# Kernel tuning notes

Hardware: AMD Instinct MI355X
Metric: run time of the kernel (lower is better)

Reference implementation:

```python
import itertools
import jax, jax.numpy as jnp
import numpy as np

N = 400000
CIN, COUT = 32, 64
K, STRIDE, PAD, DIL = 3, 2, 1, 1
SPATIAL = (200, 200, 16)
PRUNING_RATIO = 0.5

def _out_spatial():
    return tuple((s + 2 * PAD - DIL * (K - 1) - 1) // STRIDE + 1 for s in SPATIAL)


def setup_inputs() -> dict:
    key = jax.random.key(0)
    kf, kc0, kc1, kc2, kc3, km, kw = jax.random.split(key, 7)
    features = jax.random.normal(kf, (N, CIN), dtype=jnp.float32)
    b = jax.random.randint(kc0, (N,), 0, 2, dtype=jnp.int32)
    z = jax.random.randint(kc1, (N,), 0, SPATIAL[0], dtype=jnp.int32)
    y = jax.random.randint(kc2, (N,), 0, SPATIAL[1], dtype=jnp.int32)
    x = jax.random.randint(kc3, (N,), 0, SPATIAL[2], dtype=jnp.int32)
    coors = jnp.stack([b, z, y, x], axis=1)  # [N,4] = (batch, d0, d1, d2)
    mask = jax.random.uniform(km, (N,), dtype=jnp.float32)
    weight = jax.random.normal(kw, (K, K, K, CIN, COUT), dtype=jnp.float32) * 0.05
    return {"features": features, "coors": coors, "mask": mask, "weight": weight, "batch_size": 2}


def _sprs_conv(features, coors, mask, weight, batch_size):
    out_sp = _out_spatial()  # (100, 100, 8)
    num_out = batch_size * out_sp[0] * out_sp[1] * out_sp[2]
    n = features.shape[0]
    # rank-based pruning: keep top (1 - pruning_ratio) points as 'important'
    thr = jnp.sort(mask)[int(n * PRUNING_RATIO)]
    important = (mask >= thr)  # [N] bool

    b = coors[:, 0]
    pos = coors[:, 1:4]  # [N,3]
    out_sp_arr = jnp.array(out_sp, dtype=pos.dtype)

    # accumulators; slot num_out is a dump for invalid indices
    acc = jnp.zeros((num_out + 1, COUT), dtype=features.dtype)
    imp_cnt = jnp.zeros((num_out + 1,), dtype=jnp.int32)

    for off in itertools.product(range(K), repeat=3):
        off_arr = jnp.array(off, dtype=pos.dtype)
        num = pos + PAD - DIL * off_arr  # [N,3]
        oc = num // STRIDE
        valid = jnp.all(num % STRIDE == 0, axis=-1) & jnp.all(oc >= 0, axis=-1) & jnp.all(oc < out_sp_arr, axis=-1)
        lin = ((b * out_sp[0] + oc[:, 0]) * out_sp[1] + oc[:, 1]) * out_sp[2] + oc[:, 2]
        idx = jnp.where(valid, lin, num_out)
        vals = features @ weight[off[0], off[1], off[2]]  # [N,Cout] gather-GEMM
        acc = acc.at[idx].add(vals)  # scatter
        imp_cnt = imp_cnt.at[idx].add((important & valid).astype(jnp.int32))

    keep = (imp_cnt[:num_out] > 0)  # output positions reached by >=1 important point
    return acc[:num_out] * keep[:, None]


def reference(features, coors, mask, weight, batch_size):
    return _sprs_conv(features, coors, mask, weight, batch_size)
```

## Files before the change

### kernel.cpp

```cpp
#include <hip/hip_runtime.h>

#define CIN 32
#define COUT 64
#define OD0 100
#define OD1 100
#define OD2 8
#define IZ 200
#define IY 200
#define IX 16
#define NTAP 27
#define NCELLS (2 * IZ * IY * IX)
#define TOY 4
#define TOX 8
#define NROW 27
#define NCELL_R (NROW * 16)
#define NBIN 12
#define CAPB 80
#define CAPF 176


__global__ void hist0_fused_kernel(const float* __restrict__ mask, const int* __restrict__ coors,
                                   const float* __restrict__ W, int n,
                                   int* __restrict__ hist, int* __restrict__ S,
                                   float* __restrict__ Wt) {
    __shared__ int h[256];
    h[threadIdx.x] = 0;
    __syncthreads();
    for (int i = blockIdx.x * blockDim.x + threadIdx.x; i < n; i += gridDim.x * blockDim.x) {
        unsigned bits = __float_as_uint(mask[i]);
        atomicAdd(&h[bits >> 24], 1);
        const int4 c = ((const int4*)coors)[i];
        int cell = ((c.x * IZ + c.y) * IY + c.z) * IX + c.w;
        atomicAdd(&S[cell], 1);
    }
    for (int i = blockIdx.x * blockDim.x + threadIdx.x; i < NTAP * CIN * COUT;
         i += gridDim.x * blockDim.x) {
        int cout = i % COUT;
        int rest = i / COUT;
        int cin = rest % CIN;
        int tap = rest / CIN;
        Wt[((size_t)tap * COUT + cout) * CIN + cin] = W[i];
    }
    __syncthreads();
    int v = h[threadIdx.x];
    if (v) atomicAdd(&hist[threadIdx.x], v);
}

__global__ void hist8_kernel(const float* __restrict__ mask, int n, int level,
                             const int* __restrict__ state, int* __restrict__ hist) {
    __shared__ int h[256];
    h[threadIdx.x] = 0;
    __syncthreads();
    unsigned pfx = (unsigned)state[0];
    int sh = 24 - 8 * level;
    for (int i = blockIdx.x * blockDim.x + threadIdx.x; i < n; i += gridDim.x * blockDim.x) {
        unsigned bits = __float_as_uint(mask[i]);
        if ((bits >> (sh + 8)) == pfx)
            atomicAdd(&h[(bits >> sh) & 0xFF], 1);
    }
    __syncthreads();
    int v = h[threadIdx.x];
    if (v) atomicAdd(&hist[threadIdx.x], v);
}

__global__ void select8_kernel(const int* __restrict__ hist, int* __restrict__ state,
                               int level, int rankConst) {
    __shared__ int sc[256];
    sc[threadIdx.x] = hist[threadIdx.x];
    __syncthreads();
    if (threadIdx.x == 0) {
        int rank = level ? state[1] : rankConst;
        unsigned pfx = level ? (unsigned)state[0] : 0u;
        int c = 0;
        for (int j = 0; j < 256; j++) {
            int hv = sc[j];
            if (rank < c + hv) {
                state[0] = (int)((pfx << 8) | (unsigned)j);
                state[1] = rank - c;
                break;
            }
            c += hv;
        }
    }
}


__global__ void scan_l0_kernel(int* __restrict__ S, int* __restrict__ partials) {
    __shared__ int ts[256];
    int tid = threadIdx.x;
    int4 v = ((int4*)S)[blockIdx.x * 256 + tid];
    int s1 = v.x + v.y, s2 = s1 + v.z, s3 = s2 + v.w;
    ts[tid] = s3;
    __syncthreads();
    for (int off = 1; off < 256; off <<= 1) {
        int t = (tid >= off) ? ts[tid - off] : 0;
        __syncthreads();
        ts[tid] += t;
        __syncthreads();
    }
    int excl = ts[tid] - s3;
    int4 o;
    o.x = excl; o.y = excl + v.x; o.z = excl + s1; o.w = excl + s2;
    ((int4*)S)[blockIdx.x * 256 + tid] = o;
    if (tid == 255) partials[blockIdx.x] = ts[255];
}

__global__ void scan_l1_kernel(int* __restrict__ partials, int nP) {
    __shared__ int sums[256];
    int tid = threadIdx.x;
    int per = (nP + 255) / 256;
    int lo = tid * per, hi = lo + per;
    if (hi > nP) hi = nP;
    int s = 0;
    for (int j = lo; j < hi; j++) s += partials[j];
    sums[tid] = s;
    __syncthreads();
    for (int off = 1; off < 256; off <<= 1) {
        int t = (tid >= off) ? sums[tid - off] : 0;
        __syncthreads();
        sums[tid] += t;
        __syncthreads();
    }
    int run = sums[tid] - s;
    for (int j = lo; j < hi; j++) { int v = partials[j]; partials[j] = run; run += v; }
}

__global__ void scan_l2_kernel(int* __restrict__ S, const int* __restrict__ partials) {
    int add = partials[blockIdx.x];
    if (add == 0) return;
    int4 v = ((int4*)S)[blockIdx.x * 256 + threadIdx.x];
    v.x += add; v.y += add; v.z += add; v.w += add;
    ((int4*)S)[blockIdx.x * 256 + threadIdx.x] = v;
}

__global__ void scatter_points_kernel(const int* __restrict__ coors, const float* __restrict__ mask,
                                      const int* __restrict__ state, int n,
                                      int* __restrict__ S, int* __restrict__ entries) {
    int i = blockIdx.x * blockDim.x + threadIdx.x;
    if (i >= n) return;
    const int4 c = ((const int4*)coors)[i];
    int cell = ((c.x * IZ + c.y) * IY + c.z) * IX + c.w;
    float thr = __uint_as_float((unsigned)state[0]);
    int imp = (mask[i] >= thr) ? 1 : 0;
    int pos = atomicAdd(&S[cell], 1);
    entries[pos] = (i << 1) | imp;
}


__global__ void __launch_bounds__(256)
conv_kernel(const float* __restrict__ feat, const float* __restrict__ Wt,
            const int* __restrict__ S, const int* __restrict__ entries,
            float* __restrict__ out) {
    __shared__ float accS[TOY * TOX][COUT];
    __shared__ float featL[CAPF][CIN];
    __shared__ int   sLds[NROW][17];
    __shared__ unsigned work[NBIN][CAPB];
    __shared__ int   cnt[NBIN];
    __shared__ int   keepS[TOY * TOX];
    __shared__ int   nPts;
    __shared__ int   notDone;

    int tid = threadIdx.x;
    int w = tid >> 6;
    int lane = tid & 63;

    int tile = blockIdx.x;
    int oyT = (tile % (OD1 / TOY)) * TOY;
    int rest = tile / (OD1 / TOY);
    int oz = rest % OD0;
    int bb = rest / OD0;

    {
        float4 z = make_float4(0.f, 0.f, 0.f, 0.f);
        float4* a4 = (float4*)&accS[0][0];
        a4[tid] = z;
        a4[tid + 256] = z;
        if (tid < TOY * TOX) keepS[tid] = 0;
    }

    for (int idx = tid; idx < NROW * 17; idx += 256) {
        int row = idx / 17, j = idx % 17;
        int plane = row / 9, pyL = row % 9;
        int pz = 2 * oz - 1 + plane;
        int py = 2 * oyT - 1 + pyL;
        int v = 0;
        if (pz >= 0 && py >= 0) {
            int cellFlat = ((bb * IZ + pz) * IY + py) * IX + (j - 1);
            if (cellFlat >= 0) v = S[cellFlat];
        }
        sLds[row][j] = v;
    }

    int ci = tid;
    int pi = -1;

    for (;;) {
        if (tid < NBIN) cnt[tid] = 0;
        if (tid == 0) { nPts = 0; notDone = 0; }
        __syncthreads();

        while (ci < NCELL_R) {
            int row = ci >> 4, px = ci & 15;
            int rs = (pi < 0) ? sLds[row][px] : pi;
            int re = sLds[row][px + 1];
            int plane = row / 9, pyL = row % 9;
            int bin = plane * 4 + (pyL & 1) * 2 + (px & 1);
            bool blocked = false;
            for (int i = rs; i < re; i++) {
                int pos = atomicAdd(&cnt[bin], 1);
                if (pos >= CAPB) { pi = i; blocked = true; break; }
                int slot = atomicAdd(&nPts, 1);
                if (slot >= CAPF) {
                    work[bin][pos] = 0xFFFFFFFFu;
                    pi = i; blocked = true; break;
                }
                int e = entries[i];
                work[bin][pos] = ((unsigned)slot << 9) | (unsigned)((e & 1) << 8)
                               | (unsigned)(pyL << 4) | (unsigned)px;
                const float4* fp = (const float4*)(feat + (size_t)(e >> 1) * CIN);
                float4* dst = (float4*)&featL[slot][0];
                dst[0] = fp[0]; dst[1] = fp[1]; dst[2] = fp[2]; dst[3] = fp[3];
                dst[4] = fp[4]; dst[5] = fp[5]; dst[6] = fp[6]; dst[7] = fp[7];
            }
            if (blocked) break;
            ci += 256; pi = -1;
        }
        if (ci < NCELL_R) notDone = 1;
        __syncthreads();

        for (int t = w; t < NTAP; t += 4) {
            int o0 = t / 9, r9 = t % 9, o1 = r9 / 3, o2 = r9 % 3;
            int bin = o0 * 4 + (o1 & 1) * 2 + ((o2 & 1) ^ 1);
            int nb = cnt[bin];
            if (nb > CAPB) nb = CAPB;
            if (nb == 0) continue;

            const float4* wp = (const float4*)(Wt + ((size_t)t * COUT + lane) * CIN);
            float4 w0 = wp[0], w1 = wp[1], w2 = wp[2], w3 = wp[3];
            float4 w4 = wp[4], w5 = wp[5], w6 = wp[6], w7 = wp[7];

            for (int j = 0; j < nb; j++) {
                unsigned e = work[bin][j];
                if (e == 0xFFFFFFFFu) continue;
                int pyL = (int)((e >> 4) & 15u);
                int px  = (int)(e & 15u);
                int yy = (pyL - o1) >> 1;
                if ((unsigned)yy >= (unsigned)TOY) continue;
                int ox = (px + 1 - o2) >> 1;
                if ((unsigned)ox >= (unsigned)TOX) continue;

                const float4* fl = (const float4*)&featL[e >> 9][0];
                float4 f0 = fl[0], f1 = fl[1], f2 = fl[2], f3 = fl[3];
                float4 f4 = fl[4], f5 = fl[5], f6 = fl[6], f7 = fl[7];
                float a0 = 0.f, a1 = 0.f, a2 = 0.f, a3 = 0.f;
                a0 = fmaf(f0.x, w0.x, a0); a0 = fmaf(f0.y, w0.y, a0);
                a0 = fmaf(f0.z, w0.z, a0); a0 = fmaf(f0.w, w0.w, a0);
                a1 = fmaf(f1.x, w1.x, a1); a1 = fmaf(f1.y, w1.y, a1);
                a1 = fmaf(f1.z, w1.z, a1); a1 = fmaf(f1.w, w1.w, a1);
                a2 = fmaf(f2.x, w2.x, a2); a2 = fmaf(f2.y, w2.y, a2);
                a2 = fmaf(f2.z, w2.z, a2); a2 = fmaf(f2.w, w2.w, a2);
                a3 = fmaf(f3.x, w3.x, a3); a3 = fmaf(f3.y, w3.y, a3);
                a3 = fmaf(f3.z, w3.z, a3); a3 = fmaf(f3.w, w3.w, a3);
                a0 = fmaf(f4.x, w4.x, a0); a0 = fmaf(f4.y, w4.y, a0);
                a0 = fmaf(f4.z, w4.z, a0); a0 = fmaf(f4.w, w4.w, a0);
                a1 = fmaf(f5.x, w5.x, a1); a1 = fmaf(f5.y, w5.y, a1);
                a1 = fmaf(f5.z, w5.z, a1); a1 = fmaf(f5.w, w5.w, a1);
                a2 = fmaf(f6.x, w6.x, a2); a2 = fmaf(f6.y, w6.y, a2);
                a2 = fmaf(f6.z, w6.z, a2); a2 = fmaf(f6.w, w6.w, a2);
                a3 = fmaf(f7.x, w7.x, a3); a3 = fmaf(f7.y, w7.y, a3);
                a3 = fmaf(f7.z, w7.z, a3); a3 = fmaf(f7.w, w7.w, a3);

                int cl = yy * TOX + ox;
                atomicAdd(&accS[cl][lane], (a0 + a1) + (a2 + a3));
                if (lane == 0 && (e & 0x100u)) keepS[cl] = 1;
            }
        }
        __syncthreads();
        if (!notDone) break;
    }

#pragma unroll
    for (int k = 0; k < 8; k++) {
        int cl = w * 8 + k;
        int oy = oyT + (cl >> 3);
        int ox = cl & 7;
        size_t cellG = (((size_t)bb * OD0 + oz) * OD1 + oy) * OD2 + ox;
        out[cellG * COUT + lane] = keepS[cl] ? accS[cl][lane] : 0.f;
    }
}


__global__ void __launch_bounds__(256)
scatter_kernel(const float* __restrict__ feat, const int* __restrict__ coors,
               const float* __restrict__ mask, const float* __restrict__ W,
               const int* __restrict__ state, float* __restrict__ out,
               int* __restrict__ keep, int n) {
    int gid = blockIdx.x * blockDim.x + threadIdx.x;
    int wave = gid >> 6;
    int lane = threadIdx.x & 63;
    if (wave >= n) return;

    const int4 c4 = ((const int4*)coors)[wave];
    int bb = c4.x, pz = c4.y, py = c4.z, px = c4.w;

    float thr = __uint_as_float((unsigned)state[0]);
    bool imp = mask[wave] >= thr;

    int oz[2], ozo[2], nz = 0;
    int oy[2], oyo[2], ny = 0;
    int ox[2], oxo[2], nx = 0;
#pragma unroll
    for (int o = 0; o < 3; o++) {
        int num = pz + 1 - o;
        if (num >= 0 && !(num & 1) && (num >> 1) < OD0) { oz[nz] = num >> 1; ozo[nz] = o; nz++; }
        num = py + 1 - o;
        if (num >= 0 && !(num & 1) && (num >> 1) < OD1) { oy[ny] = num >> 1; oyo[ny] = o; ny++; }
        num = px + 1 - o;
        if (num >= 0 && !(num & 1) && (num >> 1) < OD2) { ox[nx] = num >> 1; oxo[nx] = o; nx++; }
    }

    float f[CIN];
    const float4* fp = (const float4*)(feat + (size_t)wave * CIN);
#pragma unroll
    for (int j = 0; j < CIN / 4; j++) {
        float4 v = fp[j];
        f[4 * j + 0] = v.x; f[4 * j + 1] = v.y; f[4 * j + 2] = v.z; f[4 * j + 3] = v.w;
    }

    for (int a = 0; a < nz; a++)
        for (int b = 0; b < ny; b++)
            for (int c = 0; c < nx; c++) {
                int woff = ((ozo[a] * 3 + oyo[b]) * 3 + oxo[c]) * (CIN * COUT);
                const float* wcol = W + woff + lane;
                float acc = 0.f;
#pragma unroll
                for (int k = 0; k < CIN; k++) acc = fmaf(f[k], wcol[k * COUT], acc);
                int lin = ((bb * OD0 + oz[a]) * OD1 + oy[b]) * OD2 + ox[c];
                atomicAdd(out + (size_t)lin * COUT + lane, acc);
                if (imp && lane == 0) keep[lin] = 1;
            }
}

__global__ void finalize_kernel(float* __restrict__ out, const int* __restrict__ keep, int numOut) {
    int t = blockIdx.x * blockDim.x + threadIdx.x;
    if (t >= numOut * (COUT / 4)) return;
    int o = t >> 4;
    if (!keep[o]) ((float4*)out)[t] = make_float4(0.f, 0.f, 0.f, 0.f);
}

extern "C" void kernel_launch(void* const* d_in, const int* in_sizes, int n_in,
                              void* d_out, int out_size, void* d_ws, size_t ws_size,
                              hipStream_t stream) {
    const float* feat  = (const float*)d_in[0];
    const int*   coors = (const int*)d_in[1];
    const float* mask  = (const float*)d_in[2];
    const float* W     = (const float*)d_in[3];

    int n = in_sizes[2];
    int numOut = out_size / COUT;
    int rank = (int)(n * 0.5);

    const int blk = 256;
    int gN = (n + blk - 1) / blk;

    char* ws = (char*)d_ws;

    size_t offHist    = 0;
    size_t offState   = 4 * 256 * 4;
    size_t offS       = offState + 64;
    size_t offPart    = offS + (size_t)NCELLS * 4;
    size_t offEntries = offPart + 1280 * 4;
    size_t offWt      = offEntries + (size_t)n * 4;
    size_t need       = offWt + (size_t)NTAP * CIN * COUT * 4;

    int* hist  = (int*)(ws + offHist);
    int* state = (int*)(ws + offState);

    if (ws_size >= need) {
        int*   S       = (int*)(ws + offS);
        int*   part    = (int*)(ws + offPart);
        int*   entries = (int*)(ws + offEntries);
        float* Wt      = (float*)(ws + offWt);

        hipMemsetAsync(ws, 0, offS + (size_t)NCELLS * 4, stream);

        hist0_fused_kernel<<<256, blk, 0, stream>>>(mask, coors, W, n, hist, S, Wt);
        select8_kernel<<<1, 256, 0, stream>>>(hist, state, 0, rank);
        for (int lvl = 1; lvl < 4; lvl++) {
            hist8_kernel<<<256, blk, 0, stream>>>(mask, n, lvl, state, hist + lvl * 256);
            select8_kernel<<<1, 256, 0, stream>>>(hist + lvl * 256, state, lvl, rank);
        }

        int nBlocksScan = NCELLS / 1024;
        scan_l0_kernel<<<nBlocksScan, 256, 0, stream>>>(S, part);
        scan_l1_kernel<<<1, 256, 0, stream>>>(part, nBlocksScan);
        scan_l2_kernel<<<nBlocksScan, 256, 0, stream>>>(S, part);
        scatter_points_kernel<<<gN, blk, 0, stream>>>(coors, mask, state, n, S, entries);

        int nTiles = numOut / (TOY * TOX);
        conv_kernel<<<nTiles, 256, 0, stream>>>(feat, Wt, S, entries, (float*)d_out);
    } else {
        int* keep = (int*)(ws + offS);
        hipMemsetAsync(d_out, 0, (size_t)out_size * sizeof(float), stream);
        hipMemsetAsync(ws, 0, offS + (size_t)numOut * 4, stream);

        hist0_fused_kernel<<<256, blk, 0, stream>>>(mask, coors, W, n, hist,
                                                    (int*)(ws + offS), (float*)(ws + offS));
        select8_kernel<<<1, 256, 0, stream>>>(hist, state, 0, rank);
        for (int lvl = 1; lvl < 4; lvl++) {
            hist8_kernel<<<256, blk, 0, stream>>>(mask, n, lvl, state, hist + lvl * 256);
            select8_kernel<<<1, 256, 0, stream>>>(hist + lvl * 256, state, lvl, rank);
        }

        long long threads = (long long)n * 64;
        int gScatter = (int)((threads + blk - 1) / blk);
        scatter_kernel<<<gScatter, blk, 0, stream>>>(feat, coors, mask, W, state,
                                                     (float*)d_out, keep, n);

        int fin = numOut * (COUT / 4);
        finalize_kernel<<<(fin + blk - 1) / blk, blk, 0, stream>>>((float*)d_out, keep, numOut);
    }
}
```

Measured before the change: 762.9 us.

## Fuse preamble into one cooperative kernel and read features directly in conv

Replaces the memset, histogram/select radix passes, three-level scan, and point scatter with a single cooperative-groups kernel that uses grid syncs between phases. The goal is to remove about a dozen kernel launches and their serialization gaps. The conv kernel also drops LDS staging of point features: it packs entry ids into the work list and loads features straight from global memory in the tap loop. Invalid contributions are routed to a dump accumulator row instead of being skipped by branches. This trades LDS capacity and branches for redundant global feature loads per tap, plus grid-sync costs.

```diff
diff --git a/kernel.cpp b/kernel.cpp
--- a/kernel.cpp
+++ b/kernel.cpp
@@ -1,4 +1,7 @@
 #include <hip/hip_runtime.h>
+#include <hip/hip_cooperative_groups.h>
+
+namespace cg = cooperative_groups;
 
 #define CIN 32
 #define COUT 64
@@ -15,8 +18,153 @@
 #define NROW 27
 #define NCELL_R (NROW * 16)
 #define NBIN 12
-#define CAPB 80
-#define CAPF 176
+#define CAPB 64
+
+#define ALOAD(p)     __hip_atomic_load((p), __ATOMIC_RELAXED, __HIP_MEMORY_SCOPE_AGENT)
+#define ASTORE(p, v) __hip_atomic_store((p), (v), __ATOMIC_RELAXED, __HIP_MEMORY_SCOPE_AGENT)
+
+
+__global__ void __launch_bounds__(256)
+preamble_kernel(const float* __restrict__ mask, const int* __restrict__ coors,
+                const float* __restrict__ W, int n, int rank,
+                int* __restrict__ hist, int* __restrict__ state,
+                int* __restrict__ S, int* __restrict__ part,
+                int* __restrict__ entries, float* __restrict__ Wt) {
+    cg::grid_group g = cg::this_grid();
+    __shared__ int h[256];
+    __shared__ int sums[256];
+    int tid = threadIdx.x, bid = blockIdx.x;
+    int gtid = bid * 256 + tid;
+    int gsz = gridDim.x * 256;
+
+    for (int i = gtid; i < NCELLS; i += gsz) S[i] = 0;
+    for (int i = gtid; i < 4 * 256; i += gsz) hist[i] = 0;
+    for (int i = gtid; i < NTAP * CIN * COUT; i += gsz) {
+        int cout = i % COUT;
+        int rest = i / COUT;
+        int cin = rest % CIN;
+        int tap = rest / CIN;
+        Wt[((size_t)tap * COUT + cout) * CIN + cin] = W[i];
+    }
+    __threadfence();
+    g.sync();
+
+    for (int lvl = 0; lvl < 4; lvl++) {
+        h[tid] = 0;
+        __syncthreads();
+        int sh = 24 - 8 * lvl;
+        unsigned pfx = lvl ? (unsigned)ALOAD(&state[0]) : 0u;
+        if (lvl == 0) {
+            for (int i = gtid; i < n; i += gsz) {
+                unsigned bits = __float_as_uint(mask[i]);
+                atomicAdd(&h[bits >> 24], 1);
+                const int4 c = ((const int4*)coors)[i];
+                atomicAdd(&S[((c.x * IZ + c.y) * IY + c.z) * IX + c.w], 1);
+            }
+        } else {
+            for (int i = gtid; i < n; i += gsz) {
+                unsigned bits = __float_as_uint(mask[i]);
+                if ((bits >> (sh + 8)) == pfx) atomicAdd(&h[(bits >> sh) & 0xFF], 1);
+            }
+        }
+        __syncthreads();
+        if (h[tid]) atomicAdd(&hist[lvl * 256 + tid], h[tid]);
+        __threadfence();
+        g.sync();
+
+        if (bid == 0) {
+            sums[tid] = ALOAD(&hist[lvl * 256 + tid]);
+            __syncthreads();
+            if (tid == 0) {
+                int rk = lvl ? state[1] : rank;
+                unsigned p2 = lvl ? (unsigned)state[0] : 0u;
+                int c = 0;
+                for (int j = 0; j < 256; j++) {
+                    int hv = sums[j];
+                    if (rk < c + hv) {
+                        ASTORE(&state[0], (int)((p2 << 8) | (unsigned)j));
+                        ASTORE(&state[1], rk - c);
+                        break;
+                    }
+                    c += hv;
+                }
+            }
+            __syncthreads();
+        }
+        __threadfence();
+        g.sync();
+    }
+
+    int nChunks = NCELLS / 1024;
+    for (int ch = bid; ch < nChunks; ch += gridDim.x) {
+        int base = ch * 1024 + tid * 4;
+        int vx = ALOAD(&S[base + 0]);
+        int vy = ALOAD(&S[base + 1]);
+        int vz = ALOAD(&S[base + 2]);
+        int vw = ALOAD(&S[base + 3]);
+        int s1 = vx + vy, s2 = s1 + vz, s3 = s2 + vw;
+        sums[tid] = s3;
+        __syncthreads();
+        for (int off = 1; off < 256; off <<= 1) {
+            int t2 = (tid >= off) ? sums[tid - off] : 0;
+            __syncthreads();
+            sums[tid] += t2;
+            __syncthreads();
+        }
+        int excl = sums[tid] - s3;
+        int4 o;
+        o.x = excl; o.y = excl + vx; o.z = excl + s1; o.w = excl + s2;
+        ((int4*)S)[ch * 256 + tid] = o;
+        if (tid == 255) ASTORE(&part[ch], sums[255]);
+        __syncthreads();
+    }
+    __threadfence();
+    g.sync();
+
+    if (bid == 0) {
+        int per = (nChunks + 255) / 256;
+        int lo = tid * per, hi = lo + per;
+        if (hi > nChunks) hi = nChunks;
+        int s = 0;
+        for (int j = lo; j < hi; j++) s += ALOAD(&part[j]);
+        sums[tid] = s;
+        __syncthreads();
+        for (int off = 1; off < 256; off <<= 1) {
+            int t2 = (tid >= off) ? sums[tid - off] : 0;
+            __syncthreads();
+            sums[tid] += t2;
+            __syncthreads();
+        }
+        int run = sums[tid] - s;
+        for (int j = lo; j < hi; j++) {
+            int v = ALOAD(&part[j]);
+            ASTORE(&part[j], run);
+            run += v;
+        }
+    }
+    __threadfence();
+    g.sync();
+
+    for (int ch = bid; ch < nChunks; ch += gridDim.x) {
+        int add = ALOAD(&part[ch]);
+        if (add != 0) {
+            int4 v = ((int4*)S)[ch * 256 + tid];
+            v.x += add; v.y += add; v.z += add; v.w += add;
+            ((int4*)S)[ch * 256 + tid] = v;
+        }
+    }
+    __threadfence();
+    g.sync();
+
+    float thr = __uint_as_float((unsigned)ALOAD(&state[0]));
+    for (int i = gtid; i < n; i += gsz) {
+        const int4 c = ((const int4*)coors)[i];
+        int cell = ((c.x * IZ + c.y) * IY + c.z) * IX + c.w;
+        int imp = (mask[i] >= thr) ? 1 : 0;
+        int pos = atomicAdd(&S[cell], 1);
+        entries[pos] = (i << 1) | imp;
+    }
+}
 
 
 __global__ void hist0_fused_kernel(const float* __restrict__ mask, const int* __restrict__ coors,
@@ -30,8 +178,7 @@
         unsigned bits = __float_as_uint(mask[i]);
         atomicAdd(&h[bits >> 24], 1);
         const int4 c = ((const int4*)coors)[i];
-        int cell = ((c.x * IZ + c.y) * IY + c.z) * IX + c.w;
-        atomicAdd(&S[cell], 1);
+        atomicAdd(&S[((c.x * IZ + c.y) * IY + c.z) * IX + c.w], 1);
     }
     for (int i = blockIdx.x * blockDim.x + threadIdx.x; i < NTAP * CIN * COUT;
          i += gridDim.x * blockDim.x) {
@@ -83,7 +230,6 @@
         }
     }
 }
-
 
 __global__ void scan_l0_kernel(int* __restrict__ S, int* __restrict__ partials) {
     __shared__ int ts[256];
@@ -151,13 +297,11 @@
 conv_kernel(const float* __restrict__ feat, const float* __restrict__ Wt,
             const int* __restrict__ S, const int* __restrict__ entries,
             float* __restrict__ out) {
-    __shared__ float accS[TOY * TOX][COUT];
-    __shared__ float featL[CAPF][CIN];
+    __shared__ float accS[TOY * TOX + 1][COUT];
     __shared__ int   sLds[NROW][17];
     __shared__ unsigned work[NBIN][CAPB];
     __shared__ int   cnt[NBIN];
     __shared__ int   keepS[TOY * TOX];
-    __shared__ int   nPts;
     __shared__ int   notDone;
 
     int tid = threadIdx.x;
@@ -173,8 +317,7 @@
     {
         float4 z = make_float4(0.f, 0.f, 0.f, 0.f);
         float4* a4 = (float4*)&accS[0][0];
-        a4[tid] = z;
-        a4[tid + 256] = z;
+        for (int i = tid; i < (TOY * TOX + 1) * (COUT / 4); i += 256) a4[i] = z;
         if (tid < TOY * TOX) keepS[tid] = 0;
     }
 
@@ -196,7 +339,7 @@
 
     for (;;) {
         if (tid < NBIN) cnt[tid] = 0;
-        if (tid == 0) { nPts = 0; notDone = 0; }
+        if (tid == 0) notDone = 0;
         __syncthreads();
 
         while (ci < NCELL_R) {
@@ -209,24 +352,15 @@
             for (int i = rs; i < re; i++) {
                 int pos = atomicAdd(&cnt[bin], 1);
                 if (pos >= CAPB) { pi = i; blocked = true; break; }
-                int slot = atomicAdd(&nPts, 1);
-                if (slot >= CAPF) {
-                    work[bin][pos] = 0xFFFFFFFFu;
-                    pi = i; blocked = true; break;
-                }
-                int e = entries[i];
-                work[bin][pos] = ((unsigned)slot << 9) | (unsigned)((e & 1) << 8)
-                               | (unsigned)(pyL << 4) | (unsigned)px;
-                const float4* fp = (const float4*)(feat + (size_t)(e >> 1) * CIN);
-                float4* dst = (float4*)&featL[slot][0];
-                dst[0] = fp[0]; dst[1] = fp[1]; dst[2] = fp[2]; dst[3] = fp[3];
-                dst[4] = fp[4]; dst[5] = fp[5]; dst[6] = fp[6]; dst[7] = fp[7];
+                unsigned e = (unsigned)entries[i];
+                work[bin][pos] = (e << 8) | (unsigned)(pyL << 4) | (unsigned)px;
             }
             if (blocked) break;
             ci += 256; pi = -1;
         }
         if (ci < NCELL_R) notDone = 1;
         __syncthreads();
+        int more = notDone;
 
         for (int t = w; t < NTAP; t += 4) {
             int o0 = t / 9, r9 = t % 9, o1 = r9 / 3, o2 = r9 % 3;
@@ -239,19 +373,20 @@
             float4 w0 = wp[0], w1 = wp[1], w2 = wp[2], w3 = wp[3];
             float4 w4 = wp[4], w5 = wp[5], w6 = wp[6], w7 = wp[7];
 
+#pragma unroll 2
             for (int j = 0; j < nb; j++) {
                 unsigned e = work[bin][j];
-                if (e == 0xFFFFFFFFu) continue;
                 int pyL = (int)((e >> 4) & 15u);
                 int px  = (int)(e & 15u);
                 int yy = (pyL - o1) >> 1;
-                if ((unsigned)yy >= (unsigned)TOY) continue;
                 int ox = (px + 1 - o2) >> 1;
-                if ((unsigned)ox >= (unsigned)TOX) continue;
-
-                const float4* fl = (const float4*)&featL[e >> 9][0];
-                float4 f0 = fl[0], f1 = fl[1], f2 = fl[2], f3 = fl[3];
-                float4 f4 = fl[4], f5 = fl[5], f6 = fl[6], f7 = fl[7];
+                bool valid = ((unsigned)yy < (unsigned)TOY) & ((unsigned)ox < (unsigned)TOX);
+                int cl = valid ? (yy * TOX + ox) : (TOY * TOX);
+                int pid = (int)(e >> 9);
+
+                const float4* fp = (const float4*)(feat + (size_t)pid * CIN);
+                float4 f0 = fp[0], f1 = fp[1], f2 = fp[2], f3 = fp[3];
+                float4 f4 = fp[4], f5 = fp[5], f6 = fp[6], f7 = fp[7];
                 float a0 = 0.f, a1 = 0.f, a2 = 0.f, a3 = 0.f;
                 a0 = fmaf(f0.x, w0.x, a0); a0 = fmaf(f0.y, w0.y, a0);
                 a0 = fmaf(f0.z, w0.z, a0); a0 = fmaf(f0.w, w0.w, a0);
@@ -270,13 +405,12 @@
                 a3 = fmaf(f7.x, w7.x, a3); a3 = fmaf(f7.y, w7.y, a3);
                 a3 = fmaf(f7.z, w7.z, a3); a3 = fmaf(f7.w, w7.w, a3);
 
-                int cl = yy * TOX + ox;
                 atomicAdd(&accS[cl][lane], (a0 + a1) + (a2 + a3));
-                if (lane == 0 && (e & 0x100u)) keepS[cl] = 1;
-            }
-        }
-        __syncthreads();
-        if (!notDone) break;
+                if (valid && lane == 0 && (e & 0x100u)) keepS[cl] = 1;
+            }
+        }
+        __syncthreads();
+        if (!more) break;
     }
 
 #pragma unroll
@@ -348,6 +482,7 @@
     if (!keep[o]) ((float4*)out)[t] = make_float4(0.f, 0.f, 0.f, 0.f);
 }
 
+
 extern "C" void kernel_launch(void* const* d_in, const int* in_sizes, int n_in,
                               void* d_out, int out_size, void* d_ws, size_t ws_size,
                               hipStream_t stream) {
@@ -382,20 +517,27 @@
         int*   entries = (int*)(ws + offEntries);
         float* Wt      = (float*)(ws + offWt);
 
-        hipMemsetAsync(ws, 0, offS + (size_t)NCELLS * 4, stream);
-
-        hist0_fused_kernel<<<256, blk, 0, stream>>>(mask, coors, W, n, hist, S, Wt);
-        select8_kernel<<<1, 256, 0, stream>>>(hist, state, 0, rank);
-        for (int lvl = 1; lvl < 4; lvl++) {
-            hist8_kernel<<<256, blk, 0, stream>>>(mask, n, lvl, state, hist + lvl * 256);
-            select8_kernel<<<1, 256, 0, stream>>>(hist + lvl * 256, state, lvl, rank);
-        }
-
-        int nBlocksScan = NCELLS / 1024;
-        scan_l0_kernel<<<nBlocksScan, 256, 0, stream>>>(S, part);
-        scan_l1_kernel<<<1, 256, 0, stream>>>(part, nBlocksScan);
-        scan_l2_kernel<<<nBlocksScan, 256, 0, stream>>>(S, part);
-        scatter_points_kernel<<<gN, blk, 0, stream>>>(coors, mask, state, n, S, entries);
+        void* args[] = { (void*)&mask, (void*)&coors, (void*)&W, (void*)&n, (void*)&rank,
+                         (void*)&hist, (void*)&state, (void*)&S, (void*)&part,
+                         (void*)&entries, (void*)&Wt };
+        hipError_t ce = hipLaunchCooperativeKernel(
+            reinterpret_cast<void*>(preamble_kernel),
+            dim3(256), dim3(256), args, 0, stream);
+
+        if (ce != hipSuccess) {
+            hipMemsetAsync(ws, 0, offS + (size_t)NCELLS * 4, stream);
+            hist0_fused_kernel<<<256, blk, 0, stream>>>(mask, coors, W, n, hist, S, Wt);
+            select8_kernel<<<1, 256, 0, stream>>>(hist, state, 0, rank);
+            for (int lvl = 1; lvl < 4; lvl++) {
+                hist8_kernel<<<256, blk, 0, stream>>>(mask, n, lvl, state, hist + lvl * 256);
+                select8_kernel<<<1, 256, 0, stream>>>(hist + lvl * 256, state, lvl, rank);
+            }
+            int nBlocksScan = NCELLS / 1024;
+            scan_l0_kernel<<<nBlocksScan, 256, 0, stream>>>(S, part);
+            scan_l1_kernel<<<1, 256, 0, stream>>>(part, nBlocksScan);
+            scan_l2_kernel<<<nBlocksScan, 256, 0, stream>>>(S, part);
+            scatter_points_kernel<<<gN, blk, 0, stream>>>(coors, mask, state, n, S, entries);
+        }
 
         int nTiles = numOut / (TOY * TOX);
         conv_kernel<<<nTiles, 256, 0, stream>>>(feat, Wt, S, entries, (float*)d_out);
@@ -404,8 +546,9 @@
         hipMemsetAsync(d_out, 0, (size_t)out_size * sizeof(float), stream);
         hipMemsetAsync(ws, 0, offS + (size_t)numOut * 4, stream);
 
+        float* WtDummy = (float*)(ws + offS);
         hist0_fused_kernel<<<256, blk, 0, stream>>>(mask, coors, W, n, hist,
-                                                    (int*)(ws + offS), (float*)(ws + offS));
+                                                    (int*)(ws + offS), WtDummy);
         select8_kernel<<<1, 256, 0, stream>>>(hist, state, 0, rank);
         for (int lvl = 1; lvl < 4; lvl++) {
             hist8_kernel<<<256, blk, 0, stream>>>(mask, n, lvl, state, hist + lvl * 256);
```

Result: slower. 1.306 ms (+71.2%).

## Restructure conv tile so each wave owns one output row, dropping LDS feature staging

Applied to the files above, without the earlier changes.

The conv kernel now bins points per input row and x-parity (54 bins) and gives each wave exclusive ownership of one output row. Accumulation becomes plain LDS adds without atomics, and the keep flags live in a per-thread bitmask. Features are read straight from global memory per tap instead of being staged in LDS, which saves LDS space and the staging copies but repeats global or cache reads for each tap. The fallback path gets a simpler histogram kernel with no S or Wt side work.

```diff
diff --git a/kernel.cpp b/kernel.cpp
--- a/kernel.cpp
+++ b/kernel.cpp
@@ -14,9 +14,8 @@
 #define TOX 8
 #define NROW 27
 #define NCELL_R (NROW * 16)
-#define NBIN 12
-#define CAPB 80
-#define CAPF 176
+#define NBIN 54
+#define CAPB 24
 
 
 __global__ void hist0_fused_kernel(const float* __restrict__ mask, const int* __restrict__ coors,
@@ -30,8 +29,7 @@
         unsigned bits = __float_as_uint(mask[i]);
         atomicAdd(&h[bits >> 24], 1);
         const int4 c = ((const int4*)coors)[i];
-        int cell = ((c.x * IZ + c.y) * IY + c.z) * IX + c.w;
-        atomicAdd(&S[cell], 1);
+        atomicAdd(&S[((c.x * IZ + c.y) * IY + c.z) * IX + c.w], 1);
     }
     for (int i = blockIdx.x * blockDim.x + threadIdx.x; i < NTAP * CIN * COUT;
          i += gridDim.x * blockDim.x) {
@@ -40,6 +38,19 @@
         int cin = rest % CIN;
         int tap = rest / CIN;
         Wt[((size_t)tap * COUT + cout) * CIN + cin] = W[i];
+    }
+    __syncthreads();
+    int v = h[threadIdx.x];
+    if (v) atomicAdd(&hist[threadIdx.x], v);
+}
+
+__global__ void hist0_simple_kernel(const float* __restrict__ mask, int n, int* __restrict__ hist) {
+    __shared__ int h[256];
+    h[threadIdx.x] = 0;
+    __syncthreads();
+    for (int i = blockIdx.x * blockDim.x + threadIdx.x; i < n; i += gridDim.x * blockDim.x) {
+        unsigned bits = __float_as_uint(mask[i]);
+        atomicAdd(&h[bits >> 24], 1);
     }
     __syncthreads();
     int v = h[threadIdx.x];
@@ -151,13 +162,10 @@
 conv_kernel(const float* __restrict__ feat, const float* __restrict__ Wt,
             const int* __restrict__ S, const int* __restrict__ entries,
             float* __restrict__ out) {
-    __shared__ float accS[TOY * TOX][COUT];
-    __shared__ float featL[CAPF][CIN];
+    __shared__ float accS[TOY][TOX][COUT];
     __shared__ int   sLds[NROW][17];
     __shared__ unsigned work[NBIN][CAPB];
     __shared__ int   cnt[NBIN];
-    __shared__ int   keepS[TOY * TOX];
-    __shared__ int   nPts;
     __shared__ int   notDone;
 
     int tid = threadIdx.x;
@@ -172,10 +180,8 @@
 
     {
         float4 z = make_float4(0.f, 0.f, 0.f, 0.f);
-        float4* a4 = (float4*)&accS[0][0];
-        a4[tid] = z;
-        a4[tid + 256] = z;
-        if (tid < TOY * TOX) keepS[tid] = 0;
+        float4* a4 = (float4*)&accS[w][0][0];
+        for (int i = lane; i < TOX * COUT / 4; i += 64) a4[i] = z;
     }
 
     for (int idx = tid; idx < NROW * 17; idx += 256) {
@@ -193,99 +199,91 @@
 
     int ci = tid;
     int pi = -1;
+    int keepMask = 0;
 
     for (;;) {
         if (tid < NBIN) cnt[tid] = 0;
-        if (tid == 0) { nPts = 0; notDone = 0; }
+        if (tid == 0) notDone = 0;
         __syncthreads();
 
         while (ci < NCELL_R) {
             int row = ci >> 4, px = ci & 15;
             int rs = (pi < 0) ? sLds[row][px] : pi;
             int re = sLds[row][px + 1];
-            int plane = row / 9, pyL = row % 9;
-            int bin = plane * 4 + (pyL & 1) * 2 + (px & 1);
+            int bin = row * 2 + (px & 1);
             bool blocked = false;
             for (int i = rs; i < re; i++) {
                 int pos = atomicAdd(&cnt[bin], 1);
                 if (pos >= CAPB) { pi = i; blocked = true; break; }
-                int slot = atomicAdd(&nPts, 1);
-                if (slot >= CAPF) {
-                    work[bin][pos] = 0xFFFFFFFFu;
-                    pi = i; blocked = true; break;
-                }
-                int e = entries[i];
-                work[bin][pos] = ((unsigned)slot << 9) | (unsigned)((e & 1) << 8)
-                               | (unsigned)(pyL << 4) | (unsigned)px;
-                const float4* fp = (const float4*)(feat + (size_t)(e >> 1) * CIN);
-                float4* dst = (float4*)&featL[slot][0];
-                dst[0] = fp[0]; dst[1] = fp[1]; dst[2] = fp[2]; dst[3] = fp[3];
-                dst[4] = fp[4]; dst[5] = fp[5]; dst[6] = fp[6]; dst[7] = fp[7];
+                unsigned e = (unsigned)entries[i];
+                work[bin][pos] = (e << 4) | (unsigned)px;
             }
             if (blocked) break;
             ci += 256; pi = -1;
         }
         if (ci < NCELL_R) notDone = 1;
         __syncthreads();
-
-        for (int t = w; t < NTAP; t += 4) {
-            int o0 = t / 9, r9 = t % 9, o1 = r9 / 3, o2 = r9 % 3;
-            int bin = o0 * 4 + (o1 & 1) * 2 + ((o2 & 1) ^ 1);
-            int nb = cnt[bin];
-            if (nb > CAPB) nb = CAPB;
-            if (nb == 0) continue;
-
-            const float4* wp = (const float4*)(Wt + ((size_t)t * COUT + lane) * CIN);
-            float4 w0 = wp[0], w1 = wp[1], w2 = wp[2], w3 = wp[3];
-            float4 w4 = wp[4], w5 = wp[5], w6 = wp[6], w7 = wp[7];
-
-            for (int j = 0; j < nb; j++) {
-                unsigned e = work[bin][j];
-                if (e == 0xFFFFFFFFu) continue;
-                int pyL = (int)((e >> 4) & 15u);
-                int px  = (int)(e & 15u);
-                int yy = (pyL - o1) >> 1;
-                if ((unsigned)yy >= (unsigned)TOY) continue;
-                int ox = (px + 1 - o2) >> 1;
-                if ((unsigned)ox >= (unsigned)TOX) continue;
-
-                const float4* fl = (const float4*)&featL[e >> 9][0];
-                float4 f0 = fl[0], f1 = fl[1], f2 = fl[2], f3 = fl[3];
-                float4 f4 = fl[4], f5 = fl[5], f6 = fl[6], f7 = fl[7];
-                float a0 = 0.f, a1 = 0.f, a2 = 0.f, a3 = 0.f;
-                a0 = fmaf(f0.x, w0.x, a0); a0 = fmaf(f0.y, w0.y, a0);
-                a0 = fmaf(f0.z, w0.z, a0); a0 = fmaf(f0.w, w0.w, a0);
-                a1 = fmaf(f1.x, w1.x, a1); a1 = fmaf(f1.y, w1.y, a1);
-                a1 = fmaf(f1.z, w1.z, a1); a1 = fmaf(f1.w, w1.w, a1);
-                a2 = fmaf(f2.x, w2.x, a2); a2 = fmaf(f2.y, w2.y, a2);
-                a2 = fmaf(f2.z, w2.z, a2); a2 = fmaf(f2.w, w2.w, a2);
-                a3 = fmaf(f3.x, w3.x, a3); a3 = fmaf(f3.y, w3.y, a3);
-                a3 = fmaf(f3.z, w3.z, a3); a3 = fmaf(f3.w, w3.w, a3);
-                a0 = fmaf(f4.x, w4.x, a0); a0 = fmaf(f4.y, w4.y, a0);
-                a0 = fmaf(f4.z, w4.z, a0); a0 = fmaf(f4.w, w4.w, a0);
-                a1 = fmaf(f5.x, w5.x, a1); a1 = fmaf(f5.y, w5.y, a1);
-                a1 = fmaf(f5.z, w5.z, a1); a1 = fmaf(f5.w, w5.w, a1);
-                a2 = fmaf(f6.x, w6.x, a2); a2 = fmaf(f6.y, w6.y, a2);
-                a2 = fmaf(f6.z, w6.z, a2); a2 = fmaf(f6.w, w6.w, a2);
-                a3 = fmaf(f7.x, w7.x, a3); a3 = fmaf(f7.y, w7.y, a3);
-                a3 = fmaf(f7.z, w7.z, a3); a3 = fmaf(f7.w, w7.w, a3);
-
-                int cl = yy * TOX + ox;
-                atomicAdd(&accS[cl][lane], (a0 + a1) + (a2 + a3));
-                if (lane == 0 && (e & 0x100u)) keepS[cl] = 1;
+        int more = notDone;
+
+        for (int o1 = 0; o1 < 3; o1++) {
+            int pyL = 2 * w + o1;
+            for (int plane = 0; plane < 3; plane++) {
+                int row = plane * 9 + pyL;
+                for (int o2 = 0; o2 < 3; o2++) {
+                    int bin = row * 2 + ((o2 == 1) ? 0 : 1);
+                    int nb = cnt[bin];
+                    if (nb > CAPB) nb = CAPB;
+                    if (nb == 0) continue;
+                    int tap = plane * 9 + o1 * 3 + o2;
+                    const float4* wp = (const float4*)(Wt + ((size_t)tap * COUT + lane) * CIN);
+                    float4 w0 = wp[0], w1 = wp[1], w2 = wp[2], w3 = wp[3];
+                    float4 w4 = wp[4], w5 = wp[5], w6 = wp[6], w7 = wp[7];
+
+#pragma unroll 2
+                    for (int j = 0; j < nb; j++) {
+                        unsigned e = work[bin][j];
+                        int px = (int)(e & 15u);
+                        int ox = (px + 1 - o2) >> 1;
+                        if ((unsigned)ox >= (unsigned)TOX) continue;
+                        int pid = (int)(e >> 5);
+
+                        const float4* fp = (const float4*)(feat + (size_t)pid * CIN);
+                        float4 f0 = fp[0], f1 = fp[1], f2 = fp[2], f3 = fp[3];
+                        float4 f4 = fp[4], f5 = fp[5], f6 = fp[6], f7 = fp[7];
+                        float a0 = 0.f, a1 = 0.f, a2 = 0.f, a3 = 0.f;
+                        a0 = fmaf(f0.x, w0.x, a0); a0 = fmaf(f0.y, w0.y, a0);
+                        a0 = fmaf(f0.z, w0.z, a0); a0 = fmaf(f0.w, w0.w, a0);
+                        a1 = fmaf(f1.x, w1.x, a1); a1 = fmaf(f1.y, w1.y, a1);
+                        a1 = fmaf(f1.z, w1.z, a1); a1 = fmaf(f1.w, w1.w, a1);
+                        a2 = fmaf(f2.x, w2.x, a2); a2 = fmaf(f2.y, w2.y, a2);
+                        a2 = fmaf(f2.z, w2.z, a2); a2 = fmaf(f2.w, w2.w, a2);
+                        a3 = fmaf(f3.x, w3.x, a3); a3 = fmaf(f3.y, w3.y, a3);
+                        a3 = fmaf(f3.z, w3.z, a3); a3 = fmaf(f3.w, w3.w, a3);
+                        a0 = fmaf(f4.x, w4.x, a0); a0 = fmaf(f4.y, w4.y, a0);
+                        a0 = fmaf(f4.z, w4.z, a0); a0 = fmaf(f4.w, w4.w, a0);
+                        a1 = fmaf(f5.x, w5.x, a1); a1 = fmaf(f5.y, w5.y, a1);
+                        a1 = fmaf(f5.z, w5.z, a1); a1 = fmaf(f5.w, w5.w, a1);
+                        a2 = fmaf(f6.x, w6.x, a2); a2 = fmaf(f6.y, w6.y, a2);
+                        a2 = fmaf(f6.z, w6.z, a2); a2 = fmaf(f6.w, w6.w, a2);
+                        a3 = fmaf(f7.x, w7.x, a3); a3 = fmaf(f7.y, w7.y, a3);
+                        a3 = fmaf(f7.z, w7.z, a3); a3 = fmaf(f7.w, w7.w, a3);
+
+                        accS[w][ox][lane] += (a0 + a1) + (a2 + a3);
+                        keepMask |= (int)((e >> 4) & 1u) << ox;
+                    }
+                }
             }
         }
         __syncthreads();
-        if (!notDone) break;
-    }
-
+        if (!more) break;
+    }
+
+    int oy = oyT + w;
 #pragma unroll
-    for (int k = 0; k < 8; k++) {
-        int cl = w * 8 + k;
-        int oy = oyT + (cl >> 3);
-        int ox = cl & 7;
+    for (int ox = 0; ox < TOX; ox++) {
         size_t cellG = (((size_t)bb * OD0 + oz) * OD1 + oy) * OD2 + ox;
-        out[cellG * COUT + lane] = keepS[cl] ? accS[cl][lane] : 0.f;
+        float v = accS[w][ox][lane];
+        out[cellG * COUT + lane] = ((keepMask >> ox) & 1) ? v : 0.f;
     }
 }
 
@@ -348,6 +346,7 @@
     if (!keep[o]) ((float4*)out)[t] = make_float4(0.f, 0.f, 0.f, 0.f);
 }
 
+
 extern "C" void kernel_launch(void* const* d_in, const int* in_sizes, int n_in,
                               void* d_out, int out_size, void* d_ws, size_t ws_size,
                               hipStream_t stream) {
@@ -404,8 +403,7 @@
         hipMemsetAsync(d_out, 0, (size_t)out_size * sizeof(float), stream);
         hipMemsetAsync(ws, 0, offS + (size_t)numOut * 4, stream);
 
-        hist0_fused_kernel<<<256, blk, 0, stream>>>(mask, coors, W, n, hist,
-                                                    (int*)(ws + offS), (float*)(ws + offS));
+        hist0_simple_kernel<<<256, blk, 0, stream>>>(mask, n, hist);
         select8_kernel<<<1, 256, 0, stream>>>(hist, state, 0, rank);
         for (int lvl = 1; lvl < 4; lvl++) {
             hist8_kernel<<<256, blk, 0, stream>>>(mask, n, lvl, state, hist + lvl * 256);
```

After: 946.6 us. 1.24x slower.
